# Optimization experiments

Measured on AMD Instinct MI355X. Metric: run time of the kernel, lower is better.

Reference implementation:

```python
import jax, jax.numpy as jnp
import numpy as np

N, B, D_IN, UNITS, K = 8192, 1, 2, 64, 2
F = D_IN + UNITS        # concatenated feature size per node
M = K + 1               # number of diffusion matrices (x0..xK)


def setup_inputs() -> dict:
    key = jax.random.key(0)
    k1, k2, k3, k4, k5, k6 = jax.random.split(key, 6)
    inputs = jax.random.normal(k1, (B, N * D_IN), dtype=jnp.float32)
    hx = jax.random.normal(k2, (B, N * UNITS), dtype=jnp.float32)
    adj = jax.random.uniform(k3, (N, N), dtype=jnp.float32)
    w_ru = jax.random.normal(k4, (F * M, 2 * UNITS), dtype=jnp.float32) * (2.0 / (F * M + 2 * UNITS)) ** 0.5
    b_ru = jnp.ones((2 * UNITS,), dtype=jnp.float32)  # bias_start=1.0 for gates
    w_c = jax.random.normal(k5, (F * M, UNITS), dtype=jnp.float32) * (2.0 / (F * M + UNITS)) ** 0.5
    b_c = jnp.zeros((UNITS,), dtype=jnp.float32)
    node_index = jax.random.randint(k6, (N,), 0, N)
    return {"inputs": inputs, "hx": hx, "adj": adj, "w_ru": w_ru,
            "b_ru": b_ru, "w_c": w_c, "b_c": b_c, "node_index": node_index}


def _gconv(adj_mx, inp, state, W, b, out_size):
    # inp: [B, N, D_IN], state: [B, N, UNITS]
    x = jnp.concatenate([inp, state], axis=2)              # [B, N, F]
    x0 = jnp.transpose(x, (1, 2, 0)).reshape(N, F * B)     # [N, F*B]
    xs = [x0]
    x1 = adj_mx @ x0                                       # 1-hop diffusion
    xs.append(x1)
    for _ in range(2, K + 1):                              # Chebyshev-style recurrence
        x2 = 2.0 * (adj_mx @ x1) - x0
        xs.append(x2)
        x0, x1 = x1, x2
    xk = jnp.stack(xs, 0).reshape(M, N, F, B)              # [M, N, F, B]
    xk = jnp.transpose(xk, (3, 1, 2, 0)).reshape(B * N, F * M)
    out = xk @ W + b                                       # [B*N, out_size]
    return out.reshape(B, N * out_size)


def reference(inputs, hx, adj, w_ru, b_ru, w_c, b_c, node_index):
    # square adj branch: adj_mx = ((D^-1)(A+I))^T, d_mat_inv = I (unused)
    adj2 = adj + jnp.eye(N, dtype=adj.dtype)
    d_inv = 1.0 / jnp.sum(adj2, axis=1)                    # no inf: diagonal added
    adj_mx = (adj2 * d_inv[:, None]).T
    inp = inputs.reshape(B, N, D_IN)
    h3 = hx.reshape(B, N, UNITS)
    value = jax.nn.sigmoid(_gconv(adj_mx, inp, h3, w_ru, b_ru, 2 * UNITS))
    value = value.reshape(B, N, 2 * UNITS)
    r = value[..., :UNITS].reshape(B, N * UNITS)
    u = value[..., UNITS:].reshape(B, N * UNITS)
    c = jnp.tanh(_gconv(adj_mx, inp, (r * hx).reshape(B, N, UNITS), w_c, b_c, UNITS))
    new_state = u * hx + (1.0 - u) * c                     # [B, N*UNITS]
    return new_state
```

## Files before the change

kernel.cpp:

```cpp
#include <hip/hip_runtime.h>
#include <math.h>


typedef __attribute__((ext_vector_type(4))) float f32x4;
typedef __attribute__((ext_vector_type(2))) int v2i;
typedef __attribute__((ext_vector_type(4))) int v4i;
typedef unsigned char uch;

constexpr int NN  = 8192;
constexpr int CST = 80;
constexpr int KBT = 256;
constexpr int SFT = KBT / 2;
constexpr int MCH = 4;
constexpr size_t NS    = (size_t)NN * CST;
constexpr size_t UTFS8 = (size_t)SFT * 5 * 1024;

constexpr float SC1  = 4096.f,   ISC1 = 1.f / 4096.f;
constexpr float SC2  = 262144.f, ISC2 = 1.f / 262144.f;

static __device__ __forceinline__ unsigned cvt2_fp8(float a, float b) {
  unsigned r = 0;
  asm("v_cvt_pk_fp8_f32 %0, %1, %2" : "+v"(r) : "v"(a), "v"(b));
  return r;
}
static __device__ __forceinline__ uint2 pack8_fp8(const float* tv) {
  uint2 pk;
  pk.x = cvt2_fp8(tv[0], tv[1]) | (cvt2_fp8(tv[2], tv[3]) << 16);
  pk.y = cvt2_fp8(tv[4], tv[5]) | (cvt2_fp8(tv[6], tv[7]) << 16);
  return pk;
}

static __device__ __forceinline__ void mfma_f8(f32x4& acc, v2i a, v2i b) {
  asm("v_mfma_f32_16x16x32_fp8_fp8 %0, %1, %2, %0" : "+v"(acc) : "v"(a), "v"(b));
}
static __device__ __forceinline__ v2i lo2(v4i v) { v2i r; r.x = v.x; r.y = v.y; return r; }
static __device__ __forceinline__ v2i hi2(v4i v) { v2i r; r.x = v.z; r.y = v.w; return r; }

__global__ __launch_bounds__(256, 4) void k_conv(const float* __restrict__ adj,
                                                 uch* __restrict__ adjF8,
                                                 float* __restrict__ dpart) {
  __shared__ float tile[2][32][132];
  const int kb = blockIdx.x, mc = blockIdx.y;
  const int tid = threadIdx.x;
  const int l = tid & 63, w = tid >> 6;
  const int rg = tid >> 5;
  const int cb = (tid & 31) * 4;
  const float* src = adj + ((size_t)kb * 32 + rg) * NN + (size_t)mc * 2048 + cb;
  float rs[4] = {0.f, 0.f, 0.f, 0.f};
  float4 vA[4], vB[4];

#pragma unroll
  for (int i = 0; i < 4; ++i)
    vA[i] = *(const float4*)(src + (size_t)(8 * i) * NN);

#define CONV_BODY(CH, BUF, VC, VN)                                             \
  {                                                                            \
    const int ch_ = (CH);                                                      \
    _Pragma("unroll") for (int i = 0; i < 4; ++i) {                            \
      int r = rg + 8 * i;                                                      \
      int colp = (cb + 8 * i) & 127;                                           \
      *(float4*)&tile[BUF][r][colp] = VC[i];                                   \
      rs[i] += (VC[i].x + VC[i].y) + (VC[i].z + VC[i].w);                      \
    }                                                                          \
    if (ch_ < 15) {                                                            \
      _Pragma("unroll") for (int i = 0; i < 4; ++i)                            \
          VN[i] = *(const float4*)(src + (size_t)(8 * i) * NN + (ch_ + 1) * 128); \
    }                                                                          \
    __syncthreads();                                                           \
    _Pragma("unroll") for (int h = 0; h < 2; ++h) {                            \
      int fl = w + 4 * h;                                                      \
      int mt = mc * 128 + ch_ * 8 + fl;                                        \
      int colp = (fl * 16 + (l & 15) + 8 * (l >> 4)) & 127;                    \
      float tv[8];                                                             \
      _Pragma("unroll") for (int j = 0; j < 8; ++j)                            \
        tv[j] = tile[BUF][8 * (l >> 4) + j][colp];                             \
      uint2 pk = pack8_fp8(tv);                                                \
      *(uint2*)(adjF8 + ((size_t)mt * SFT + (kb >> 1)) * 1024                  \
                + l * 16 + (kb & 1) * 8) = pk;                                 \
    }                                                                          \
  }

  for (int cp = 0; cp < 8; ++cp) {
    CONV_BODY(2 * cp,     0, vA, vB);
    CONV_BODY(2 * cp + 1, 1, vB, vA);
  }
#undef CONV_BODY

#pragma unroll
  for (int i = 0; i < 4; ++i) {
#pragma unroll
    for (int m = 16; m >= 1; m >>= 1) rs[i] += __shfl_xor(rs[i], m);
  }
  if ((tid & 31) == 0) {
#pragma unroll
    for (int i = 0; i < 4; ++i)
      dpart[(size_t)mc * NN + kb * 32 + 8 * i + rg] = rs[i];
  }
}

__global__ __launch_bounds__(256) void k_build(const float* __restrict__ hx,
                                               const float* __restrict__ inp,
                                               const float* __restrict__ dpart,
                                               float* __restrict__ dinv,
                                               float* __restrict__ X0,
                                               float* __restrict__ XS0,
                                               uch* __restrict__ UtF8) {
  __shared__ float dv_s[32];
  const int bid = blockIdx.x;
  const int n0 = bid * 32;
  const int tid = threadIdx.x;
  if (tid < 32) {
    int n = n0 + tid;
    float dv = 1.f / (dpart[n] + dpart[NN + n] + dpart[2 * NN + n] +
                      dpart[3 * NN + n] + 1.f);
    dv_s[tid] = dv;
    dinv[n] = dv;
  }
  __syncthreads();
  for (int p = tid; p < 32 * 20; p += 256) {
    int nl = p / 20, c4 = (p % 20) * 4;
    int n = n0 + nl;
    float dv = dv_s[nl];
    float v[4];
#pragma unroll
    for (int j = 0; j < 4; ++j) {
      int c = c4 + j;
      v[j] = (c < 64) ? hx[n * 64 + c] : (c < 66 ? inp[n * 2 + (c - 64)] : 0.f);
    }
    size_t o = (size_t)n * CST + c4;
    *(float4*)(X0 + o)  = make_float4(v[0], v[1], v[2], v[3]);
    *(float4*)(XS0 + o) = make_float4(dv * v[0], dv * v[1], dv * v[2], dv * v[3]);
  }
  for (int p = tid; p < 5 * 64; p += 256) {
    int nt = p >> 6, l = p & 63;
    float tv[8];
#pragma unroll
    for (int j = 0; j < 8; ++j) {
      int nloc = 8 * (l >> 4) + j;
      int n = n0 + nloc;
      int c = nt * 16 + (l & 15);
      float v = (c < 64) ? hx[n * 64 + c] : (c < 66 ? inp[n * 2 + (c - 64)] : 0.f);
      tv[j] = v * dv_s[nloc] * SC1;
    }
    uint2 pk = pack8_fp8(tv);
    *(uint2*)(UtF8 + ((size_t)(bid >> 1) * 5 + nt) * 1024 + l * 16 + (bid & 1) * 8) = pk;
  }
}

static __device__ __forceinline__ void gemm_core1(const uch* __restrict__ adjF8,
                                                  const uch* __restrict__ bF8,
                                                  int mt, int tid, float* smem,
                                                  float& sv0, float& sv1,
                                                  float& sv2, float inv_scale) {
  const int w8 = tid >> 6, l = tid & 63;
  const int sf0 = w8 * 16;
  f32x4 acc[5];
#pragma unroll
  for (int nt = 0; nt < 5; ++nt) acc[nt] = (f32x4){0.f, 0.f, 0.f, 0.f};
  const uch* ap = adjF8 + ((size_t)mt * SFT + sf0) * 1024 + l * 16;
  const uch* bp = bF8 + (size_t)sf0 * 5 * 1024 + l * 16;

  v4i Ae, Ao, Be[5], Bo[5];
  Ae = *(const v4i*)(ap);
#pragma unroll
  for (int nt = 0; nt < 5; ++nt) Be[nt] = *(const v4i*)(bp + nt * 1024);

  for (int sf = 0; sf < 16; sf += 2) {
    Ao = *(const v4i*)(ap + (size_t)(sf + 1) * 1024);
#pragma unroll
    for (int nt = 0; nt < 5; ++nt)
      Bo[nt] = *(const v4i*)(bp + (size_t)((sf + 1) * 5 + nt) * 1024);
#pragma unroll
    for (int nt = 0; nt < 5; ++nt) mfma_f8(acc[nt], lo2(Ae), lo2(Be[nt]));
#pragma unroll
    for (int nt = 0; nt < 5; ++nt) mfma_f8(acc[nt], hi2(Ae), hi2(Be[nt]));
    Ae = *(const v4i*)(ap + (size_t)(sf + 2) * 1024);
#pragma unroll
    for (int nt = 0; nt < 5; ++nt)
      Be[nt] = *(const v4i*)(bp + (size_t)((sf + 2) * 5 + nt) * 1024);
#pragma unroll
    for (int nt = 0; nt < 5; ++nt) mfma_f8(acc[nt], lo2(Ao), lo2(Bo[nt]));
#pragma unroll
    for (int nt = 0; nt < 5; ++nt) mfma_f8(acc[nt], hi2(Ao), hi2(Bo[nt]));
  }
  asm volatile("s_nop 7\n\ts_nop 7\n\ts_nop 7" ::: "memory");

  auto red = reinterpret_cast<float(*)[64][20]>(smem);
  if (w8 < 4) {
#pragma unroll
    for (int nt = 0; nt < 5; ++nt) *(f32x4*)&red[w8][l][nt * 4] = acc[nt];
  }
  __syncthreads();
  if (w8 >= 4) {
#pragma unroll
    for (int nt = 0; nt < 5; ++nt) {
      f32x4 t = *(f32x4*)&red[w8 - 4][l][nt * 4];
      *(f32x4*)&red[w8 - 4][l][nt * 4] = t + acc[nt];
    }
  }
  __syncthreads();
#define GATHER(P)                                                              \
  ({ int p_ = (P); int r_ = p_ / 80, c_ = p_ % 80;                             \
     int ll_ = ((r_ >> 2) << 4) | (c_ & 15);                                   \
     int k_ = ((c_ >> 4) << 2) | (r_ & 3);                                     \
     (((red[0][ll_][k_] + red[1][ll_][k_]) + red[2][ll_][k_])                  \
      + red[3][ll_][k_]) * inv_scale; })
  sv0 = GATHER(tid);
  sv1 = GATHER(tid + 512);
  sv2 = (tid < 256) ? GATHER(tid + 1024) : 0.f;
#undef GATHER
  __syncthreads();
}

#define UTF_WRITE_HALF(DST, VALEXPR, SCALE)                                    \
  {                                                                            \
    const int sfK = mt >> 2;                                                   \
    const int byteoff = ((mt >> 1) & 1) * 8;                                   \
    const int lbase = (mt & 1) * 32;                                           \
    for (int p = tid; p < 5 * 32; p += 512) {                                  \
      int nt = p >> 5, idx = p & 31;                                           \
      int l2 = lbase + idx;                                                    \
      float tv_[8];                                                            \
      _Pragma("unroll") for (int j = 0; j < 8; ++j) {                          \
        int lr = 8 * (idx >> 4) + j;                                           \
        int cc = nt * 16 + (idx & 15);                                         \
        tv_[j] = (VALEXPR) * (SCALE);                                          \
      }                                                                        \
      uint2 pk = pack8_fp8(tv_);                                               \
      *(uint2*)((DST) + ((size_t)sfK * 5 + nt) * 1024 + l2 * 16 + byteoff) = pk; \
    }                                                                          \
  }

__global__ __launch_bounds__(512, 4) void k_hop1(const uch* __restrict__ adjF8,
                                                 const uch* __restrict__ UtFin,
                                                 const float* __restrict__ XSin,
                                                 const float* __restrict__ dinv,
                                                 float* __restrict__ X1,
                                                 float* __restrict__ XS1,
                                                 uch* __restrict__ UtFout) {
  __shared__ __align__(16) float smem[5120];
  const int mt = blockIdx.x, tid = threadIdx.x;
  const int n0 = mt * 16;
  float sv0, sv1, sv2;
  gemm_core1(adjF8, UtFin, mt, tid, smem, sv0, sv1, sv2, ISC1);

  auto xs = reinterpret_cast<float(*)[80]>(smem);
#define HOP1_ITEM(P, SV)                                                       \
  { int p_ = (P); size_t o_ = (size_t)n0 * CST + p_;                           \
    float x1_ = XSin[o_] + (SV);                                               \
    X1[o_] = x1_;                                                              \
    float z_ = dinv[n0 + p_ / 80] * x1_;                                       \
    XS1[o_] = z_;                                                              \
    xs[p_ / 80][p_ % 80] = z_; }
  HOP1_ITEM(tid, sv0)
  HOP1_ITEM(tid + 512, sv1)
  if (tid < 256) HOP1_ITEM(tid + 1024, sv2)
#undef HOP1_ITEM
  __syncthreads();
  UTF_WRITE_HALF(UtFout, xs[lr][cc], SC2)
}

__global__ __launch_bounds__(512, 4) void k_hop2g(const uch* __restrict__ adjF8,
    const uch* __restrict__ UtFb, const float* __restrict__ XS1,
    const float* __restrict__ X0, const float* __restrict__ X1,
    const float* __restrict__ w_ru, const float* __restrict__ b_ru,
    const float* __restrict__ hx, const float* __restrict__ inp,
    const float* __restrict__ dinv,
    float* __restrict__ X0w, float* __restrict__ XS0w,
    uch* __restrict__ UtFa, float* __restrict__ UG) {
  __shared__ __align__(16) float smem[5120];
  const int mt = blockIdx.x, tid = threadIdx.x;
  const int n0 = mt * 16;
  float sv0, sv1, sv2;
  gemm_core1(adjF8, UtFb, mt, tid, smem, sv0, sv1, sv2, ISC2);

  auto xr2 = reinterpret_cast<float(*)[80]>(smem);
  float* xr01 = smem + 1280;
  float* rhq  = smem + 1280 + 2176;
#define X2_ITEM(P, SV)                                                         \
  { int p_ = (P); size_t o_ = (size_t)n0 * CST + p_;                           \
    xr2[p_ / 80][p_ % 80] = 2.f * (XS1[o_] + (SV)) - X0[o_]; }
  X2_ITEM(tid, sv0)
  X2_ITEM(tid + 512, sv1)
  if (tid < 256) X2_ITEM(tid + 1024, sv2)
#undef X2_ITEM
  for (int p = tid; p < 16 * 17; p += 512) {
    int nl = p / 17, c4 = (p % 17) * 4;
    size_t o = (size_t)(n0 + nl) * CST + c4;
    *(float4*)&xr01[nl * 68 + c4]            = *(const float4*)(X0 + o);
    *(float4*)&xr01[16 * 68 + nl * 68 + c4]  = *(const float4*)(X1 + o);
  }
  __syncthreads();

  const int nl = tid >> 5, og = tid & 31, o0 = og * 4;
  float acc[4];
#pragma unroll
  for (int j = 0; j < 4; ++j) acc[j] = b_ru[o0 + j];
  for (int c = 0; c < 66; ++c) {
    int f = (c < 64) ? (c + 2) : (c - 64);
    const float* wr = w_ru + (size_t)(f * 3) * 128 + o0;
    float xv[3];
    xv[0] = xr01[nl * 68 + c];
    xv[1] = xr01[16 * 68 + nl * 68 + c];
    xv[2] = xr2[nl][c];
#pragma unroll
    for (int m = 0; m < 3; ++m) {
      float wl[4];
      *(float4*)(wl) = *(const float4*)(wr + m * 128);
#pragma unroll
      for (int j = 0; j < 4; ++j) acc[j] += xv[m] * wl[j];
    }
  }
  const int n = n0 + nl;
  const float dv = dinv[n];
  if (og < 16) {
#pragma unroll
    for (int j = 0; j < 4; ++j) {
      int o = o0 + j;
      float r = 1.f / (1.f + expf(-acc[j]));
      float rh = r * hx[n * 64 + o];
      X0w[(size_t)n * CST + o] = rh;
      float srh = dv * rh;
      XS0w[(size_t)n * CST + o] = srh;
      rhq[nl * 64 + o] = srh;
    }
  } else {
#pragma unroll
    for (int j = 0; j < 4; ++j)
      UG[n * 64 + (o0 - 64) + j] = 1.f / (1.f + expf(-acc[j]));
  }
  __syncthreads();
  UTF_WRITE_HALF(UtFa,
                 (cc < 64) ? rhq[lr * 64 + cc]
                           : ((cc < 66) ? dinv[n0 + lr] * inp[(n0 + lr) * 2 + (cc - 64)]
                                        : 0.f),
                 SC1)
}

__global__ __launch_bounds__(512, 4) void k_hop2f(const uch* __restrict__ adjF8,
    const uch* __restrict__ UtFb, const float* __restrict__ XS1,
    const float* __restrict__ X0, const float* __restrict__ X1,
    const float* __restrict__ w_c, const float* __restrict__ b_c,
    const float* __restrict__ hx, const float* __restrict__ UG,
    float* __restrict__ out) {
  __shared__ __align__(16) float smem[5120];
  const int mt = blockIdx.x, tid = threadIdx.x;
  const int n0 = mt * 16;
  float sv0, sv1, sv2;
  gemm_core1(adjF8, UtFb, mt, tid, smem, sv0, sv1, sv2, ISC2);

  auto xr2 = reinterpret_cast<float(*)[80]>(smem);
  float* xr01 = smem + 1280;
#define X2_ITEM(P, SV)                                                         \
  { int p_ = (P); size_t o_ = (size_t)n0 * CST + p_;                           \
    xr2[p_ / 80][p_ % 80] = 2.f * (XS1[o_] + (SV)) - X0[o_]; }
  X2_ITEM(tid, sv0)
  X2_ITEM(tid + 512, sv1)
  if (tid < 256) X2_ITEM(tid + 1024, sv2)
#undef X2_ITEM
  for (int p = tid; p < 16 * 17; p += 512) {
    int nl = p / 17, c4 = (p % 17) * 4;
    size_t o = (size_t)(n0 + nl) * CST + c4;
    *(float4*)&xr01[nl * 68 + c4]           = *(const float4*)(X0 + o);
    *(float4*)&xr01[16 * 68 + nl * 68 + c4] = *(const float4*)(X1 + o);
  }
  __syncthreads();

  const int nl = tid >> 5, ot = tid & 31, o0 = ot * 2;
  float acc[2];
#pragma unroll
  for (int j = 0; j < 2; ++j) acc[j] = b_c[o0 + j];
  for (int c = 0; c < 66; ++c) {
    int f = (c < 64) ? (c + 2) : (c - 64);
    float xv[3];
    xv[0] = xr01[nl * 68 + c];
    xv[1] = xr01[16 * 68 + nl * 68 + c];
    xv[2] = xr2[nl][c];
#pragma unroll
    for (int m = 0; m < 3; ++m) {
      float wl[2];
      *(float2*)(wl) = *(const float2*)(w_c + (size_t)(f * 3 + m) * 64 + o0);
#pragma unroll
      for (int j = 0; j < 2; ++j) acc[j] += xv[m] * wl[j];
    }
  }
  const int n = n0 + nl;
#pragma unroll
  for (int j = 0; j < 2; ++j) {
    int o = o0 + j;
    float cc = tanhf(acc[j]);
    float u = UG[n * 64 + o];
    float h = hx[n * 64 + o];
    out[n * 64 + o] = u * h + (1.f - u) * cc;
  }
}

extern "C" void kernel_launch(void* const* d_in, const int* in_sizes, int n_in,
                              void* d_out, int out_size, void* d_ws, size_t ws_size,
                              hipStream_t stream) {
  const float* inp  = (const float*)d_in[0];
  const float* hx   = (const float*)d_in[1];
  const float* adj  = (const float*)d_in[2];
  const float* w_ru = (const float*)d_in[3];
  const float* b_ru = (const float*)d_in[4];
  const float* w_c  = (const float*)d_in[5];
  const float* b_c  = (const float*)d_in[6];
  float* out = (float*)d_out;

  float* ws    = (float*)d_ws;
  float* dinv  = ws;
  float* dpart = ws + 8192;
  float* X0    = ws + 8192 + 4 * 8192;
  float* XS0   = X0 + NS;
  float* X1    = XS0 + NS;
  float* XS1   = X1 + NS;
  uch* UtFa8   = (uch*)(XS1 + NS);
  uch* UtFb8   = UtFa8 + UTFS8;
  uch* adjF8   = UtFb8 + UTFS8;
  float* UG    = (float*)(adjF8 + (size_t)512 * SFT * 1024);

  dim3 cg(KBT, MCH);

  k_conv <<<cg, 256, 0, stream>>>(adj, adjF8, dpart);
  k_build<<<NN / 32, 256, 0, stream>>>(hx, inp, dpart, dinv, X0, XS0, UtFa8);

  k_hop1 <<<512, 512, 0, stream>>>(adjF8, UtFa8, XS0, dinv, X1, XS1, UtFb8);
  k_hop2g<<<512, 512, 0, stream>>>(adjF8, UtFb8, XS1, X0, X1, w_ru, b_ru, hx, inp,
                                   dinv, X0, XS0, UtFa8, UG);

  k_hop1 <<<512, 512, 0, stream>>>(adjF8, UtFa8, XS0, dinv, X1, XS1, UtFb8);
  k_hop2f<<<512, 512, 0, stream>>>(adjF8, UtFb8, XS1, X0, X1, w_c, b_c, hx, UG, out);
}
```

Baseline: 212.9 us.

## Store diffusion intermediates as bf16 and recompute scaled copies from dinv

Replaces the fp32 X0/XS0/X1/XS1 workspace arrays with two bf16 arrays (X0b, X1b). The dinv-scaled copies are no longer stored; each kernel recomputes them by multiplying by dinv on the fly. This halves the element width and drops half the arrays, cutting global write and read traffic in the hop kernels. The cost is bf16 rounding of intermediates that were fp32, a small accuracy risk. The old k_hop2f is left in place with a stub dinv of 1, and a new k_hop2f2 that takes the real dinv is launched instead.

```diff
diff --git a/kernel.cpp b/kernel.cpp
--- a/kernel.cpp
+++ b/kernel.cpp
@@ -6,6 +6,7 @@
 typedef __attribute__((ext_vector_type(2))) int v2i;
 typedef __attribute__((ext_vector_type(4))) int v4i;
 typedef unsigned char uch;
+typedef unsigned short ush;
 
 constexpr int NN  = 8192;
 constexpr int CST = 80;
@@ -17,6 +18,16 @@
 
 constexpr float SC1  = 4096.f,   ISC1 = 1.f / 4096.f;
 constexpr float SC2  = 262144.f, ISC2 = 1.f / 262144.f;
+
+static __device__ __forceinline__ float bf2f(ush u) {
+  union { float f; unsigned v; } c; c.v = ((unsigned)u) << 16; return c.f;
+}
+static __device__ __forceinline__ ush f2bf(float x) {
+  union { float f; unsigned u; } c; c.f = x;
+  unsigned u = c.u;
+  u += 0x7fffu + ((u >> 16) & 1u);
+  return (ush)(u >> 16);
+}
 
 static __device__ __forceinline__ unsigned cvt2_fp8(float a, float b) {
   unsigned r = 0;
@@ -102,8 +113,7 @@
                                                const float* __restrict__ inp,
                                                const float* __restrict__ dpart,
                                                float* __restrict__ dinv,
-                                               float* __restrict__ X0,
-                                               float* __restrict__ XS0,
+                                               ush* __restrict__ X0b,
                                                uch* __restrict__ UtF8) {
   __shared__ float dv_s[32];
   const int bid = blockIdx.x;
@@ -120,16 +130,16 @@
   for (int p = tid; p < 32 * 20; p += 256) {
     int nl = p / 20, c4 = (p % 20) * 4;
     int n = n0 + nl;
-    float dv = dv_s[nl];
     float v[4];
 #pragma unroll
     for (int j = 0; j < 4; ++j) {
       int c = c4 + j;
       v[j] = (c < 64) ? hx[n * 64 + c] : (c < 66 ? inp[n * 2 + (c - 64)] : 0.f);
     }
-    size_t o = (size_t)n * CST + c4;
-    *(float4*)(X0 + o)  = make_float4(v[0], v[1], v[2], v[3]);
-    *(float4*)(XS0 + o) = make_float4(dv * v[0], dv * v[1], dv * v[2], dv * v[3]);
+    uint2 pk;
+    pk.x = f2bf(v[0]) | ((unsigned)f2bf(v[1]) << 16);
+    pk.y = f2bf(v[2]) | ((unsigned)f2bf(v[3]) << 16);
+    *(uint2*)(X0b + (size_t)n * CST + c4) = pk;
   }
   for (int p = tid; p < 5 * 64; p += 256) {
     int nt = p >> 6, l = p & 63;
@@ -233,10 +243,9 @@
 
 __global__ __launch_bounds__(512, 4) void k_hop1(const uch* __restrict__ adjF8,
                                                  const uch* __restrict__ UtFin,
-                                                 const float* __restrict__ XSin,
+                                                 const ush* __restrict__ X0b,
                                                  const float* __restrict__ dinv,
-                                                 float* __restrict__ X1,
-                                                 float* __restrict__ XS1,
+                                                 ush* __restrict__ X1b,
                                                  uch* __restrict__ UtFout) {
   __shared__ __align__(16) float smem[5120];
   const int mt = blockIdx.x, tid = threadIdx.x;
@@ -247,11 +256,10 @@
   auto xs = reinterpret_cast<float(*)[80]>(smem);
 #define HOP1_ITEM(P, SV)                                                       \
   { int p_ = (P); size_t o_ = (size_t)n0 * CST + p_;                           \
-    float x1_ = XSin[o_] + (SV);                                               \
-    X1[o_] = x1_;                                                              \
-    float z_ = dinv[n0 + p_ / 80] * x1_;                                       \
-    XS1[o_] = z_;                                                              \
-    xs[p_ / 80][p_ % 80] = z_; }
+    float dv_ = dinv[n0 + p_ / 80];                                            \
+    float x1_ = dv_ * bf2f(X0b[o_]) + (SV);                                    \
+    X1b[o_] = f2bf(x1_);                                                       \
+    xs[p_ / 80][p_ % 80] = dv_ * x1_; }
   HOP1_ITEM(tid, sv0)
   HOP1_ITEM(tid + 512, sv1)
   if (tid < 256) HOP1_ITEM(tid + 1024, sv2)
@@ -261,12 +269,11 @@
 }
 
 __global__ __launch_bounds__(512, 4) void k_hop2g(const uch* __restrict__ adjF8,
-    const uch* __restrict__ UtFb, const float* __restrict__ XS1,
-    const float* __restrict__ X0, const float* __restrict__ X1,
+    const uch* __restrict__ UtFb, const ush* __restrict__ X1b,
+    ush* __restrict__ X0b,
     const float* __restrict__ w_ru, const float* __restrict__ b_ru,
     const float* __restrict__ hx, const float* __restrict__ inp,
     const float* __restrict__ dinv,
-    float* __restrict__ X0w, float* __restrict__ XS0w,
     uch* __restrict__ UtFa, float* __restrict__ UG) {
   __shared__ __align__(16) float smem[5120];
   const int mt = blockIdx.x, tid = threadIdx.x;
@@ -279,7 +286,9 @@
   float* rhq  = smem + 1280 + 2176;
 #define X2_ITEM(P, SV)                                                         \
   { int p_ = (P); size_t o_ = (size_t)n0 * CST + p_;                           \
-    xr2[p_ / 80][p_ % 80] = 2.f * (XS1[o_] + (SV)) - X0[o_]; }
+    float dv_ = dinv[n0 + p_ / 80];                                            \
+    xr2[p_ / 80][p_ % 80] =                                                    \
+        2.f * (dv_ * bf2f(X1b[o_]) + (SV)) - bf2f(X0b[o_]); }
   X2_ITEM(tid, sv0)
   X2_ITEM(tid + 512, sv1)
   if (tid < 256) X2_ITEM(tid + 1024, sv2)
@@ -287,8 +296,11 @@
   for (int p = tid; p < 16 * 17; p += 512) {
     int nl = p / 17, c4 = (p % 17) * 4;
     size_t o = (size_t)(n0 + nl) * CST + c4;
-    *(float4*)&xr01[nl * 68 + c4]            = *(const float4*)(X0 + o);
-    *(float4*)&xr01[16 * 68 + nl * 68 + c4]  = *(const float4*)(X1 + o);
+#pragma unroll
+    for (int j = 0; j < 4; ++j) {
+      xr01[nl * 68 + c4 + j]           = bf2f(X0b[o + j]);
+      xr01[16 * 68 + nl * 68 + c4 + j] = bf2f(X1b[o + j]);
+    }
   }
   __syncthreads();
 
@@ -319,10 +331,8 @@
       int o = o0 + j;
       float r = 1.f / (1.f + expf(-acc[j]));
       float rh = r * hx[n * 64 + o];
-      X0w[(size_t)n * CST + o] = rh;
-      float srh = dv * rh;
-      XS0w[(size_t)n * CST + o] = srh;
-      rhq[nl * 64 + o] = srh;
+      X0b[(size_t)n * CST + o] = f2bf(rh);
+      rhq[nl * 64 + o] = dv * rh;
     }
   } else {
 #pragma unroll
@@ -338,8 +348,8 @@
 }
 
 __global__ __launch_bounds__(512, 4) void k_hop2f(const uch* __restrict__ adjF8,
-    const uch* __restrict__ UtFb, const float* __restrict__ XS1,
-    const float* __restrict__ X0, const float* __restrict__ X1,
+    const uch* __restrict__ UtFb, const ush* __restrict__ X1b,
+    const ush* __restrict__ X0b,
     const float* __restrict__ w_c, const float* __restrict__ b_c,
     const float* __restrict__ hx, const float* __restrict__ UG,
     float* __restrict__ out) {
@@ -353,7 +363,11 @@
   float* xr01 = smem + 1280;
 #define X2_ITEM(P, SV)                                                         \
   { int p_ = (P); size_t o_ = (size_t)n0 * CST + p_;                           \
-    xr2[p_ / 80][p_ % 80] = 2.f * (XS1[o_] + (SV)) - X0[o_]; }
+    float dv_ = dinv_g[p_ / 80];                                               \
+    xr2[p_ / 80][p_ % 80] =                                                    \
+        2.f * (dv_ * bf2f(X1b[o_]) + (SV)) - bf2f(X0b[o_]); }
+  __shared__ float dinv_g[16];
+  if (tid < 16) dinv_g[tid] = 1.f;
   X2_ITEM(tid, sv0)
   X2_ITEM(tid + 512, sv1)
   if (tid < 256) X2_ITEM(tid + 1024, sv2)
@@ -361,8 +375,74 @@
   for (int p = tid; p < 16 * 17; p += 512) {
     int nl = p / 17, c4 = (p % 17) * 4;
     size_t o = (size_t)(n0 + nl) * CST + c4;
-    *(float4*)&xr01[nl * 68 + c4]           = *(const float4*)(X0 + o);
-    *(float4*)&xr01[16 * 68 + nl * 68 + c4] = *(const float4*)(X1 + o);
+#pragma unroll
+    for (int j = 0; j < 4; ++j) {
+      xr01[nl * 68 + c4 + j]           = bf2f(X0b[o + j]);
+      xr01[16 * 68 + nl * 68 + c4 + j] = bf2f(X1b[o + j]);
+    }
+  }
+  __syncthreads();
+
+  const int nl = tid >> 5, ot = tid & 31, o0 = ot * 2;
+  float acc[2];
+#pragma unroll
+  for (int j = 0; j < 2; ++j) acc[j] = b_c[o0 + j];
+  for (int c = 0; c < 66; ++c) {
+    int f = (c < 64) ? (c + 2) : (c - 64);
+    float xv[3];
+    xv[0] = xr01[nl * 68 + c];
+    xv[1] = xr01[16 * 68 + nl * 68 + c];
+    xv[2] = xr2[nl][c];
+#pragma unroll
+    for (int m = 0; m < 3; ++m) {
+      float wl[2];
+      *(float2*)(wl) = *(const float2*)(w_c + (size_t)(f * 3 + m) * 64 + o0);
+#pragma unroll
+      for (int j = 0; j < 2; ++j) acc[j] += xv[m] * wl[j];
+    }
+  }
+  const int n = n0 + nl;
+#pragma unroll
+  for (int j = 0; j < 2; ++j) {
+    int o = o0 + j;
+    float cc = tanhf(acc[j]);
+    float u = UG[n * 64 + o];
+    float h = hx[n * 64 + o];
+    out[n * 64 + o] = u * h + (1.f - u) * cc;
+  }
+}
+
+__global__ __launch_bounds__(512, 4) void k_hop2f2(const uch* __restrict__ adjF8,
+    const uch* __restrict__ UtFb, const ush* __restrict__ X1b,
+    const ush* __restrict__ X0b, const float* __restrict__ dinv,
+    const float* __restrict__ w_c, const float* __restrict__ b_c,
+    const float* __restrict__ hx, const float* __restrict__ UG,
+    float* __restrict__ out) {
+  __shared__ __align__(16) float smem[5120];
+  const int mt = blockIdx.x, tid = threadIdx.x;
+  const int n0 = mt * 16;
+  float sv0, sv1, sv2;
+  gemm_core1(adjF8, UtFb, mt, tid, smem, sv0, sv1, sv2, ISC2);
+
+  auto xr2 = reinterpret_cast<float(*)[80]>(smem);
+  float* xr01 = smem + 1280;
+#define X2_ITEM(P, SV)                                                         \
+  { int p_ = (P); size_t o_ = (size_t)n0 * CST + p_;                           \
+    float dv_ = dinv[n0 + p_ / 80];                                            \
+    xr2[p_ / 80][p_ % 80] =                                                    \
+        2.f * (dv_ * bf2f(X1b[o_]) + (SV)) - bf2f(X0b[o_]); }
+  X2_ITEM(tid, sv0)
+  X2_ITEM(tid + 512, sv1)
+  if (tid < 256) X2_ITEM(tid + 1024, sv2)
+#undef X2_ITEM
+  for (int p = tid; p < 16 * 17; p += 512) {
+    int nl = p / 17, c4 = (p % 17) * 4;
+    size_t o = (size_t)(n0 + nl) * CST + c4;
+#pragma unroll
+    for (int j = 0; j < 4; ++j) {
+      xr01[nl * 68 + c4 + j]           = bf2f(X0b[o + j]);
+      xr01[16 * 68 + nl * 68 + c4 + j] = bf2f(X1b[o + j]);
+    }
   }
   __syncthreads();
 
@@ -410,11 +490,9 @@
   float* ws    = (float*)d_ws;
   float* dinv  = ws;
   float* dpart = ws + 8192;
-  float* X0    = ws + 8192 + 4 * 8192;
-  float* XS0   = X0 + NS;
-  float* X1    = XS0 + NS;
-  float* XS1   = X1 + NS;
-  uch* UtFa8   = (uch*)(XS1 + NS);
+  ush* X0b     = (ush*)(ws + 8192 + 4 * 8192);
+  ush* X1b     = X0b + NS;
+  uch* UtFa8   = (uch*)(X1b + NS);
   uch* UtFb8   = UtFa8 + UTFS8;
   uch* adjF8   = UtFb8 + UTFS8;
   float* UG    = (float*)(adjF8 + (size_t)512 * SFT * 1024);
@@ -422,12 +500,13 @@
   dim3 cg(KBT, MCH);
 
   k_conv <<<cg, 256, 0, stream>>>(adj, adjF8, dpart);
-  k_build<<<NN / 32, 256, 0, stream>>>(hx, inp, dpart, dinv, X0, XS0, UtFa8);
-
-  k_hop1 <<<512, 512, 0, stream>>>(adjF8, UtFa8, XS0, dinv, X1, XS1, UtFb8);
-  k_hop2g<<<512, 512, 0, stream>>>(adjF8, UtFb8, XS1, X0, X1, w_ru, b_ru, hx, inp,
-                                   dinv, X0, XS0, UtFa8, UG);
-
-  k_hop1 <<<512, 512, 0, stream>>>(adjF8, UtFa8, XS0, dinv, X1, XS1, UtFb8);
-  k_hop2f<<<512, 512, 0, stream>>>(adjF8, UtFb8, XS1, X0, X1, w_c, b_c, hx, UG, out);
-}
+  k_build<<<NN / 32, 256, 0, stream>>>(hx, inp, dpart, dinv, X0b, UtFa8);
+
+  k_hop1 <<<512, 512, 0, stream>>>(adjF8, UtFa8, X0b, dinv, X1b, UtFb8);
+  k_hop2g<<<512, 512, 0, stream>>>(adjF8, UtFb8, X1b, X0b, w_ru, b_ru, hx, inp,
+                                   dinv, UtFa8, UG);
+
+  k_hop1 <<<512, 512, 0, stream>>>(adjF8, UtFa8, X0b, dinv, X1b, UtFb8);
+  k_hop2f2<<<512, 512, 0, stream>>>(adjF8, UtFb8, X1b, X0b, dinv, w_c, b_c, hx,
+                                    UG, out);
+}
```

Measured after the change: 210.9 us. Within noise of the previous version (-0.9%).
